# Kernel optimization log

Hardware: AMD Instinct MI355X
Metric: run time of the kernel (lower is better)

## Reference

```python
import jax, jax.numpy as jnp
import numpy as np

DIM = 1024
NUM_HEADS = 16
HEAD_DIM = DIM // NUM_HEADS
BATCH = 64
SEQ = 256


def rope_tables(seq_len, head_dim, dtype=jnp.float32):
    inv_freq = 1.0 / (10000.0 ** (jnp.arange(0, head_dim, 2, dtype=jnp.float32) / head_dim))
    pos = jnp.arange(seq_len, dtype=jnp.float32)
    freqs = jnp.outer(pos, inv_freq)            # (S, head_dim/2)
    emb = jnp.concatenate([freqs, freqs], -1)   # (S, head_dim)
    return jnp.cos(emb).astype(dtype), jnp.sin(emb).astype(dtype)


def rotate_half(x):
    x1, x2 = jnp.split(x, 2, axis=-1)
    return jnp.concatenate([-x2, x1], axis=-1)


def setup_inputs() -> dict:
    key = jax.random.key(0)
    ks = jax.random.split(key, 5)
    x = jax.random.normal(ks[0], (BATCH, SEQ, DIM), dtype=jnp.float32)
    mask = jnp.ones((BATCH, SEQ), dtype=jnp.int32)
    s = 1.0 / np.sqrt(DIM)
    Wq = jax.random.normal(ks[1], (DIM, DIM), dtype=jnp.float32) * s
    Wk = jax.random.normal(ks[2], (DIM, DIM), dtype=jnp.float32) * s
    Wv = jax.random.normal(ks[3], (DIM, DIM), dtype=jnp.float32) * s
    Wo = jax.random.normal(ks[4], (DIM, DIM), dtype=jnp.float32) * s
    return {"x": x, "mask": mask, "Wq": Wq, "Wk": Wk, "Wv": Wv, "Wo": Wo}


def reference(x, mask, Wq, Wk, Wv, Wo):
    B, S, D = x.shape
    H, Hd = NUM_HEADS, HEAD_DIM
    scale = Hd ** -0.5
    # torch nn.Linear: y = x @ W^T  (weights stored as (out,in))
    q = (x @ Wq.T).reshape(B, S, H, Hd).transpose(0, 2, 1, 3)  # (B,H,S,Hd)
    k = (x @ Wk.T).reshape(B, S, H, Hd).transpose(0, 2, 1, 3)
    v = (x @ Wv.T).reshape(B, S, H, Hd).transpose(0, 2, 1, 3)
    cos, sin = rope_tables(S, Hd, x.dtype)       # (S,Hd)
    cos = cos[None, None]                         # (1,1,S,Hd)
    sin = sin[None, None]
    q = q * cos + rotate_half(q) * sin
    k = k * cos + rotate_half(k) * sin
    scores = jnp.einsum('bhqd,bhkd->bhqk', q, k) * scale  # (B,H,S,S)
    m = (mask[:, None, None, :] != 0)             # (B,1,1,S)
    scores = jnp.where(m, scores, -jnp.inf)
    attn = jax.nn.softmax(scores, axis=-1)
    out = jnp.einsum('bhqk,bhkd->bhqd', attn, v)  # (B,H,S,Hd)
    out = out.transpose(0, 2, 1, 3).reshape(B, S, D)
    return out @ Wo.T
```

## Files before the change

### kernel.cpp

```cpp
#include <hip/hip_runtime.h>

typedef __attribute__((ext_vector_type(8))) short short8;
typedef __attribute__((ext_vector_type(4))) float f32x4;

#define DEV __device__ __forceinline__

DEV unsigned short f2bf(float f) {
    unsigned int u = __float_as_uint(f);
    u += 0x7FFFu + ((u >> 16) & 1u);
    return (unsigned short)(u >> 16);
}
DEV float bf2f(unsigned short h) { return __uint_as_float(((unsigned int)h) << 16); }

DEV void gload16(const void* g, void* l) {
    __builtin_amdgcn_global_load_lds(
        (const __attribute__((address_space(1))) void*)(unsigned long long)g,
        (__attribute__((address_space(3))) void*)(unsigned int)(unsigned long long)l,
        16, 0, 0);
}

__global__ void cast_bf16_kernel(const float* __restrict__ in, unsigned short* __restrict__ out, int n8) {
    int gid = blockIdx.x * 256 + threadIdx.x;
    if (gid >= n8) return;
    const f32x4* p = (const f32x4*)in + (size_t)gid * 2;
    f32x4 a = p[0], b = p[1];
    short8 v;
    v[0] = (short)f2bf(a[0]); v[1] = (short)f2bf(a[1]); v[2] = (short)f2bf(a[2]); v[3] = (short)f2bf(a[3]);
    v[4] = (short)f2bf(b[0]); v[5] = (short)f2bf(b[1]); v[6] = (short)f2bf(b[2]); v[7] = (short)f2bf(b[3]);
    *(short8*)(out + (size_t)gid * 8) = v;
}

__global__ void cast_w4_kernel(const float* __restrict__ w0, const float* __restrict__ w1,
                               const float* __restrict__ w2, const float* __restrict__ w3,
                               unsigned short* __restrict__ o0, unsigned short* __restrict__ o1,
                               unsigned short* __restrict__ o2, unsigned short* __restrict__ o3) {
    int gid = blockIdx.x * 256 + threadIdx.x;
    int sel = gid >> 17, idx = gid & 131071;
    const float* in = (sel == 0) ? w0 : (sel == 1) ? w1 : (sel == 2) ? w2 : w3;
    unsigned short* out = (sel == 0) ? o0 : (sel == 1) ? o1 : (sel == 2) ? o2 : o3;
    const f32x4* p = (const f32x4*)in + (size_t)idx * 2;
    f32x4 a = p[0], b = p[1];
    short8 v;
    v[0] = (short)f2bf(a[0]); v[1] = (short)f2bf(a[1]); v[2] = (short)f2bf(a[2]); v[3] = (short)f2bf(a[3]);
    v[4] = (short)f2bf(b[0]); v[5] = (short)f2bf(b[1]); v[6] = (short)f2bf(b[2]); v[7] = (short)f2bf(b[3]);
    *(short8*)(out + (size_t)idx * 8) = v;
}

__global__ void rope_table_kernel(float* __restrict__ cosT, float* __restrict__ sinT) {
    int gid = blockIdx.x * 256 + threadIdx.x;
    if (gid >= 256 * 32) return;
    int s = gid >> 5, i = gid & 31;
    float inv = powf(10000.0f, -(float)i * (1.0f / 32.0f));
    float f = (float)s * inv;
    cosT[gid] = cosf(f);
    sinT[gid] = sinf(f);
}

#define NT 32

#define STAGE(SB, TS) do {                                                     \
    int ts_ = (TS) < NT ? (TS) : (NT - 1);                                     \
    const unsigned short* as_ = Abase + (size_t)ts_ * 32;                      \
    const unsigned short* bs_ = Bbase + (size_t)ts_ * 32;                      \
    gload16(as_ + rel0, &Al[SB][(size_t)tid * 8]);                             \
    gload16(as_ + rel1, &Al[SB][(size_t)(tid + 512) * 8]);                     \
    gload16(bs_ + rel0, &Bl[SB][(size_t)tid * 8]);                             \
    gload16(bs_ + rel1, &Bl[SB][(size_t)(tid + 512) * 8]);                     \
} while (0)

#define RDB(BUF) do {                                                          \
    bv[0] = *(const short8*)&Bl[BUF][boff[0]];                                 \
    bv[1] = *(const short8*)&Bl[BUF][boff[1]];                                 \
    bv[2] = *(const short8*)&Bl[BUF][boff[2]];                                 \
    bv[3] = *(const short8*)&Bl[BUF][boff[3]];                                 \
} while (0)

#define RDA(FR, BUF) do {                                                      \
    FR[0] = *(const short8*)&Al[BUF][aoff[0]];                                 \
    FR[1] = *(const short8*)&Al[BUF][aoff[1]];                                 \
    FR[2] = *(const short8*)&Al[BUF][aoff[2]];                                 \
    FR[3] = *(const short8*)&Al[BUF][aoff[3]];                                 \
    FR[4] = *(const short8*)&Al[BUF][aoff[4]];                                 \
    FR[5] = *(const short8*)&Al[BUF][aoff[5]];                                 \
    FR[6] = *(const short8*)&Al[BUF][aoff[6]];                                 \
    FR[7] = *(const short8*)&Al[BUF][aoff[7]];                                 \
} while (0)

#define MFMA32(F) do {                                                         \
    _Pragma("unroll")                                                          \
    for (int ni = 0; ni < 4; ++ni)                                             \
        _Pragma("unroll")                                                      \
        for (int mi = 0; mi < 8; ++mi)                                         \
            acc[mi][ni] = __builtin_amdgcn_mfma_f32_16x16x32_bf16(             \
                F[mi], bv[ni], acc[mi][ni], 0, 0, 0);                          \
} while (0)

#define TILEB(T, CURB, NXTB, STB, FCUR, FNXT) do {                             \
    RDB(CURB);                                                                 \
    RDA(FNXT, NXTB);                                                           \
    STAGE(STB, (T) + 3);                                                       \
    __builtin_amdgcn_s_setprio(1);                                             \
    MFMA32(FCUR);                                                              \
    __builtin_amdgcn_s_setprio(0);                                             \
    asm volatile("s_waitcnt vmcnt(4)" ::: "memory");                           \
    __builtin_amdgcn_s_barrier();                                              \
    asm volatile("" ::: "memory");                                             \
} while (0)

template <int MODE>
__global__ __launch_bounds__(512, 2) void gemm256_kernel(
    const unsigned short* __restrict__ A,
    const unsigned short* __restrict__ W0,
    const unsigned short* __restrict__ W1,
    const unsigned short* __restrict__ W2,
    unsigned short* __restrict__ q,
    unsigned short* __restrict__ k,
    unsigned short* __restrict__ vt,
    float* __restrict__ outF,
    const float* __restrict__ cosT,
    const float* __restrict__ sinT)
{
    __shared__ __align__(16) unsigned short Al[4][8192];
    __shared__ __align__(16) unsigned short Bl[4][8192];

    const int tid = threadIdx.x;
    const int l = tid & 63;
    const int w = tid >> 6;
    const int wr = w >> 2, wc = w & 3;
    const int l15 = l & 15, lg = l >> 4;

    const int nwg = gridDim.x;
    const int bid = blockIdx.x;
    const int cpx = nwg >> 3;
    const int swz = (bid & 7) * cpx + (bid >> 3);
    const int NBX = (MODE == 0) ? 12 : 4;
    const int bx = swz % NBX, by = swz / NBX;
    const int m0 = by * 256, n0 = bx * 256;

    const unsigned short* Bp;
    int nb, sel = 0;
    if (MODE == 0) {
        sel = n0 >> 10;
        Bp = (sel == 0) ? W0 : ((sel == 1) ? W1 : W2);
        nb = n0 & 1023;
    } else {
        Bp = W0;
        nb = n0;
    }

    const int f0 = tid, f1 = tid + 512;
    const int rel0 = (f0 >> 2) * 1024 + (((f0 & 3) ^ ((f0 >> 3) & 3)) * 8);
    const int rel1 = (f1 >> 2) * 1024 + (((f1 & 3) ^ ((f1 >> 3) & 3)) * 8);
    const unsigned short* Abase = A + (size_t)m0 * 1024;
    const unsigned short* Bbase = Bp + (size_t)nb * 1024;

    int aoff[8], boff[4];
#pragma unroll
    for (int mi = 0; mi < 8; ++mi) {
        int row = wr * 128 + mi * 16 + l15;
        aoff[mi] = row * 32 + ((lg ^ ((row >> 1) & 3)) * 8);
    }
#pragma unroll
    for (int ni = 0; ni < 4; ++ni) {
        int row = wc * 64 + ni * 16 + l15;
        boff[ni] = row * 32 + ((lg ^ ((row >> 1) & 3)) * 8);
    }

    f32x4 acc[8][4];
#pragma unroll
    for (int mi = 0; mi < 8; ++mi)
#pragma unroll
        for (int ni = 0; ni < 4; ++ni)
#pragma unroll
            for (int e = 0; e < 4; ++e) acc[mi][ni][e] = 0.f;

    short8 bv[4], fA[8], fB[8];

    STAGE(0, 0);
    STAGE(1, 1);
    STAGE(2, 2);
    asm volatile("s_waitcnt vmcnt(4)" ::: "memory");
    __builtin_amdgcn_s_barrier();
    asm volatile("" ::: "memory");
    RDA(fA, 0);

#pragma unroll 1
    for (int it = 0; it < NT / 4; ++it) {
        const int t0 = it * 4;
        TILEB(t0 + 0, 0, 1, 3, fA, fB);
        TILEB(t0 + 1, 1, 2, 0, fB, fA);
        TILEB(t0 + 2, 2, 3, 1, fA, fB);
        TILEB(t0 + 3, 3, 0, 2, fB, fA);
    }

    if (MODE == 0) {
#pragma unroll
        for (int mi = 0; mi < 8; ++mi) {
#pragma unroll
            for (int i = 0; i < 4; ++i) {
                int grow = m0 + wr * 128 + mi * 16 + lg * 4 + i;
                int b = grow >> 8, s = grow & 255;
                if (sel < 2) {
#pragma unroll
                    for (int ni = 0; ni < 2; ++ni) {
                        int d = ni * 16 + l15;
                        float c = cosT[s * 32 + d], sn = sinT[s * 32 + d];
                        float lo = acc[mi][ni][i], hi = acc[mi][ni + 2][i];
                        acc[mi][ni][i] = lo * c - hi * sn;
                        acc[mi][ni + 2][i] = hi * c + lo * sn;
                    }
                }
#pragma unroll
                for (int ni = 0; ni < 4; ++ni) {
                    int col = n0 + wc * 64 + ni * 16 + l15;
                    int cc = col & 1023;
                    int h = cc >> 6, d = cc & 63;
                    unsigned short v = f2bf(acc[mi][ni][i]);
                    if (sel == 0)
                        q[((size_t)(b * 16 + h) * 256 + s) * 64 + d] = v;
                    else if (sel == 1)
                        k[((size_t)(b * 16 + h) * 256 + s) * 64 + d] = v;
                    else
                        vt[((size_t)(b * 16 + h) * 64 + d) * 256 + s] = v;
                }
            }
        }
    } else {
#pragma unroll
        for (int mi = 0; mi < 8; ++mi) {
#pragma unroll
            for (int i = 0; i < 4; ++i) {
                int grow = m0 + wr * 128 + mi * 16 + lg * 4 + i;
#pragma unroll
                for (int ni = 0; ni < 4; ++ni) {
                    int col = n0 + wc * 64 + ni * 16 + l15;
                    outF[(size_t)grow * 1024 + col] = acc[mi][ni][i];
                }
            }
        }
    }
}

__global__ __launch_bounds__(512) void attn_kernel(
    const unsigned short* __restrict__ qp,
    const unsigned short* __restrict__ kp,
    const unsigned short* __restrict__ vtp,
    const int* __restrict__ mask,
    unsigned short* __restrict__ ao)
{
    __shared__ __align__(16) unsigned short Ks[128 * 64];
    __shared__ __align__(16) unsigned short Vts[64 * 128];
    __shared__ __align__(16) unsigned short Ps[8][32 * 64];

    const int bh = blockIdx.x;
    const int b = bh >> 4, h = bh & 15;
    const int tid = threadIdx.x;
    const int l = tid & 63, w = tid >> 6;
    const int l15 = l & 15, lg = l >> 4;

    const unsigned short* kbase = kp + (size_t)bh * (256 * 64);
    const unsigned short* vtbase = vtp + (size_t)bh * (64 * 256);
    const unsigned short* qbase = qp + (size_t)bh * (256 * 64) + (size_t)(w * 32) * 64;

    short8 aq[2][2];
#pragma unroll
    for (int m = 0; m < 2; ++m)
#pragma unroll
        for (int ks = 0; ks < 2; ++ks)
            aq[m][ks] = *(const short8*)(qbase + (m * 16 + l15) * 64 + ks * 32 + lg * 8);

    float m_run[2][4], l_run[2][4];
    f32x4 o[2][4];
#pragma unroll
    for (int m = 0; m < 2; ++m)
#pragma unroll
        for (int i = 0; i < 4; ++i) { m_run[m][i] = -3.0e38f; l_run[m][i] = 0.f; }
#pragma unroll
    for (int m = 0; m < 2; ++m)
#pragma unroll
        for (int n = 0; n < 4; ++n)
#pragma unroll
            for (int e = 0; e < 4; ++e) o[m][n][e] = 0.f;

    const int* mrow = mask + b * 256;

    for (int half = 0; half < 2; ++half) {
        __syncthreads();
        for (int c2 = tid; c2 < 1024; c2 += 512) {
            int off = c2 * 16;
            int row = off >> 7, cb = off & 127;
            short8 v = *(const short8*)((const char*)kbase + (size_t)half * 16384 + off);
            *(short8*)((char*)Ks + row * 128 + (cb ^ ((row & 7) << 4))) = v;
        }
        for (int c2 = tid; c2 < 1024; c2 += 512) {
            int off = c2 * 16;
            int row = off >> 8, cb = off & 255;
            short8 v = *(const short8*)((const char*)vtbase + (size_t)row * 512 + half * 256 + cb);
            *(short8*)((char*)Vts + row * 256 + (cb ^ ((row & 7) << 4))) = v;
        }
        __syncthreads();

        for (int t2 = 0; t2 < 2; ++t2) {
            const int keyl = t2 * 64;
            const int keyg = half * 128 + keyl;

            f32x4 sf[2][4];
#pragma unroll
            for (int m = 0; m < 2; ++m)
#pragma unroll
                for (int n = 0; n < 4; ++n)
#pragma unroll
                    for (int e = 0; e < 4; ++e) sf[m][n][e] = 0.f;
#pragma unroll
            for (int ks = 0; ks < 2; ++ks) {
                short8 bk[4];
#pragma unroll
                for (int n = 0; n < 4; ++n) {
                    int row = keyl + n * 16 + l15;
                    int cb = (ks * 64 + lg * 16) ^ ((row & 7) << 4);
                    bk[n] = *(const short8*)((char*)Ks + row * 128 + cb);
                }
#pragma unroll
                for (int m = 0; m < 2; ++m)
#pragma unroll
                    for (int n = 0; n < 4; ++n)
                        sf[m][n] = __builtin_amdgcn_mfma_f32_16x16x32_bf16(aq[m][ks], bk[n], sf[m][n], 0, 0, 0);
            }
            float madd[4];
#pragma unroll
            for (int n = 0; n < 4; ++n) madd[n] = mrow[keyg + n * 16 + l15] ? 0.f : -1e30f;
#pragma unroll
            for (int m = 0; m < 2; ++m)
#pragma unroll
                for (int n = 0; n < 4; ++n)
#pragma unroll
                    for (int i = 0; i < 4; ++i) sf[m][n][i] = sf[m][n][i] * 0.125f + madd[n];
            float al[2][4];
#pragma unroll
            for (int m = 0; m < 2; ++m)
#pragma unroll
                for (int i = 0; i < 4; ++i) {
                    float mx = fmaxf(fmaxf(sf[m][0][i], sf[m][1][i]), fmaxf(sf[m][2][i], sf[m][3][i]));
                    mx = fmaxf(mx, __shfl_xor(mx, 1));
                    mx = fmaxf(mx, __shfl_xor(mx, 2));
                    mx = fmaxf(mx, __shfl_xor(mx, 4));
                    mx = fmaxf(mx, __shfl_xor(mx, 8));
                    float mnew = fmaxf(m_run[m][i], mx);
                    al[m][i] = __expf(m_run[m][i] - mnew);
                    m_run[m][i] = mnew;
                }
            float rs[2][4];
#pragma unroll
            for (int m = 0; m < 2; ++m)
#pragma unroll
                for (int i = 0; i < 4; ++i) rs[m][i] = 0.f;
#pragma unroll
            for (int m = 0; m < 2; ++m)
#pragma unroll
                for (int n = 0; n < 4; ++n)
#pragma unroll
                    for (int i = 0; i < 4; ++i) {
                        float p = __expf(sf[m][n][i] - m_run[m][i]);
                        sf[m][n][i] = p;
                        rs[m][i] += p;
                    }
#pragma unroll
            for (int m = 0; m < 2; ++m)
#pragma unroll
                for (int i = 0; i < 4; ++i) {
                    float r2 = rs[m][i];
                    r2 += __shfl_xor(r2, 1);
                    r2 += __shfl_xor(r2, 2);
                    r2 += __shfl_xor(r2, 4);
                    r2 += __shfl_xor(r2, 8);
                    l_run[m][i] = l_run[m][i] * al[m][i] + r2;
                }
#pragma unroll
            for (int m = 0; m < 2; ++m)
#pragma unroll
                for (int n = 0; n < 4; ++n)
#pragma unroll
                    for (int i = 0; i < 4; ++i) o[m][n][i] *= al[m][i];

            __syncthreads();
#pragma unroll
            for (int m = 0; m < 2; ++m)
#pragma unroll
                for (int n = 0; n < 4; ++n)
#pragma unroll
                    for (int i = 0; i < 4; ++i) {
                        int row = m * 16 + lg * 4 + i;
                        int cb = ((n * 16 + l15) * 2) ^ ((row & 7) << 4);
                        *(unsigned short*)((char*)Ps[w] + row * 128 + cb) = f2bf(sf[m][n][i]);
                    }
            __syncthreads();
#pragma unroll
            for (int ks = 0; ks < 2; ++ks) {
                short8 pa[2];
#pragma unroll
                for (int m = 0; m < 2; ++m) {
                    int row = m * 16 + l15;
                    int cb = (ks * 64 + lg * 16) ^ ((row & 7) << 4);
                    pa[m] = *(const short8*)((char*)Ps[w] + row * 128 + cb);
                }
                short8 vb[4];
#pragma unroll
                for (int n = 0; n < 4; ++n) {
                    int row = n * 16 + l15;
                    int cb = (keyl * 2 + ks * 64 + lg * 16) ^ ((row & 7) << 4);
                    vb[n] = *(const short8*)((char*)Vts + row * 256 + cb);
                }
#pragma unroll
                for (int m = 0; m < 2; ++m)
#pragma unroll
                    for (int n = 0; n < 4; ++n)
                        o[m][n] = __builtin_amdgcn_mfma_f32_16x16x32_bf16(pa[m], vb[n], o[m][n], 0, 0, 0);
            }
        }
    }

    unsigned short* aop = ao + ((size_t)(b * 256 + w * 32)) * 1024 + h * 64;
#pragma unroll
    for (int m = 0; m < 2; ++m)
#pragma unroll
        for (int n = 0; n < 4; ++n)
#pragma unroll
            for (int i = 0; i < 4; ++i) {
                int row = m * 16 + lg * 4 + i;
                int d = n * 16 + l15;
                aop[(size_t)row * 1024 + d] = f2bf(o[m][n][i] / l_run[m][i]);
            }
}

extern "C" void kernel_launch(void* const* d_in, const int* in_sizes, int n_in,
                              void* d_out, int out_size, void* d_ws, size_t ws_size,
                              hipStream_t stream) {
    const float* x = (const float*)d_in[0];
    const int* mask = (const int*)d_in[1];
    const float* Wq = (const float*)d_in[2];
    const float* Wk = (const float*)d_in[3];
    const float* Wv = (const float*)d_in[4];
    const float* Wo = (const float*)d_in[5];
    float* out = (float*)d_out;

    char* ws = (char*)d_ws;
    size_t off = 0;
    auto alloc = [&](size_t bytes) -> char* {
        char* p = ws + off;
        off = (off + bytes + 255) & ~(size_t)255;
        return p;
    };
    unsigned short* xb = (unsigned short*)alloc((size_t)16384 * 1024 * 2);
    unsigned short* wqb = (unsigned short*)alloc((size_t)1024 * 1024 * 2);
    unsigned short* wkb = (unsigned short*)alloc((size_t)1024 * 1024 * 2);
    unsigned short* wvb = (unsigned short*)alloc((size_t)1024 * 1024 * 2);
    unsigned short* wob = (unsigned short*)alloc((size_t)1024 * 1024 * 2);
    unsigned short* q = (unsigned short*)alloc((size_t)16384 * 1024 * 2);
    unsigned short* k = (unsigned short*)alloc((size_t)16384 * 1024 * 2);
    unsigned short* vt = (unsigned short*)alloc((size_t)16384 * 1024 * 2);
    float* cosT = (float*)alloc(256 * 32 * 4);
    float* sinT = (float*)alloc(256 * 32 * 4);

    cast_bf16_kernel<<<16777216 / 8 / 256, 256, 0, stream>>>(x, xb, 16777216 / 8);
    cast_w4_kernel<<<4 * 131072 / 256, 256, 0, stream>>>(Wq, Wk, Wv, Wo, wqb, wkb, wvb, wob);
    rope_table_kernel<<<32, 256, 0, stream>>>(cosT, sinT);

    gemm256_kernel<0><<<768, 512, 0, stream>>>(xb, wqb, wkb, wvb, q, k, vt, nullptr, cosT, sinT);
    attn_kernel<<<1024, 512, 0, stream>>>(q, k, vt, mask, xb );
    gemm256_kernel<1><<<256, 512, 0, stream>>>(xb, wob, nullptr, nullptr, nullptr, nullptr, nullptr, out, nullptr, nullptr);

    (void)in_sizes; (void)n_in; (void)out_size; (void)ws_size;
}
```

Measured before the change: 298.7 us.

## Restructure GEMM main loop into two half-tile phases with prefetch depth two

The GEMM K-loop now splits each K-tile into two phases of sixteen MFMAs each. Each phase reads half of the A fragments (plus B in the first phase) from LDS, issues the global-to-LDS load for only the A or only the B half of a future tile, and synchronises with barriers and sched_barrier fences. Prefetch depth drops from three tiles ahead to two, and the fB register double-buffer is removed, which cuts VGPR pressure. This interleaves memory issue with compute more finely, at the cost of extra barriers per tile and a shallower prefetch.

```diff
diff --git a/kernel.cpp b/kernel.cpp
--- a/kernel.cpp
+++ b/kernel.cpp
@@ -58,53 +58,59 @@
 
 #define NT 32
 
-#define STAGE(SB, TS) do {                                                     \
+#define RD16(ARR, OFF) (*(const short8*)&(ARR)[OFF])
+
+#define STG(DST, BASEP, TS) do {                                               \
     int ts_ = (TS) < NT ? (TS) : (NT - 1);                                     \
-    const unsigned short* as_ = Abase + (size_t)ts_ * 32;                      \
-    const unsigned short* bs_ = Bbase + (size_t)ts_ * 32;                      \
-    gload16(as_ + rel0, &Al[SB][(size_t)tid * 8]);                             \
-    gload16(as_ + rel1, &Al[SB][(size_t)(tid + 512) * 8]);                     \
-    gload16(bs_ + rel0, &Bl[SB][(size_t)tid * 8]);                             \
-    gload16(bs_ + rel1, &Bl[SB][(size_t)(tid + 512) * 8]);                     \
+    const unsigned short* sp_ = (BASEP) + (size_t)ts_ * 32;                    \
+    gload16(sp_ + rel0, &(DST)[(size_t)tid * 8]);                              \
+    gload16(sp_ + rel1, &(DST)[(size_t)(tid + 512) * 8]);                      \
 } while (0)
 
-#define RDB(BUF) do {                                                          \
-    bv[0] = *(const short8*)&Bl[BUF][boff[0]];                                 \
-    bv[1] = *(const short8*)&Bl[BUF][boff[1]];                                 \
-    bv[2] = *(const short8*)&Bl[BUF][boff[2]];                                 \
-    bv[3] = *(const short8*)&Bl[BUF][boff[3]];                                 \
+#define MM4(MI, A) do {                                                        \
+    acc[MI][0] = __builtin_amdgcn_mfma_f32_16x16x32_bf16(A, bv[0], acc[MI][0], 0, 0, 0); \
+    acc[MI][1] = __builtin_amdgcn_mfma_f32_16x16x32_bf16(A, bv[1], acc[MI][1], 0, 0, 0); \
+    acc[MI][2] = __builtin_amdgcn_mfma_f32_16x16x32_bf16(A, bv[2], acc[MI][2], 0, 0, 0); \
+    acc[MI][3] = __builtin_amdgcn_mfma_f32_16x16x32_bf16(A, bv[3], acc[MI][3], 0, 0, 0); \
 } while (0)
 
-#define RDA(FR, BUF) do {                                                      \
-    FR[0] = *(const short8*)&Al[BUF][aoff[0]];                                 \
-    FR[1] = *(const short8*)&Al[BUF][aoff[1]];                                 \
-    FR[2] = *(const short8*)&Al[BUF][aoff[2]];                                 \
-    FR[3] = *(const short8*)&Al[BUF][aoff[3]];                                 \
-    FR[4] = *(const short8*)&Al[BUF][aoff[4]];                                 \
-    FR[5] = *(const short8*)&Al[BUF][aoff[5]];                                 \
-    FR[6] = *(const short8*)&Al[BUF][aoff[6]];                                 \
-    FR[7] = *(const short8*)&Al[BUF][aoff[7]];                                 \
+#define PHA(BUF, SBUF, TS) do {                                                \
+    short8 a0 = RD16(Al[BUF], aoff[0]);                                        \
+    short8 a1 = RD16(Al[BUF], aoff[1]);                                        \
+    short8 a2 = RD16(Al[BUF], aoff[2]);                                        \
+    short8 a3 = RD16(Al[BUF], aoff[3]);                                        \
+    bv[0] = RD16(Bl[BUF], boff[0]);                                            \
+    bv[1] = RD16(Bl[BUF], boff[1]);                                            \
+    bv[2] = RD16(Bl[BUF], boff[2]);                                            \
+    bv[3] = RD16(Bl[BUF], boff[3]);                                            \
+    STG(Al[SBUF], Abase, TS);                                                  \
+    __builtin_amdgcn_sched_barrier(0);                                         \
+    __builtin_amdgcn_s_barrier();                                              \
+    asm volatile("s_waitcnt lgkmcnt(0)" ::: "memory");                         \
+    __builtin_amdgcn_sched_barrier(0);                                         \
+    __builtin_amdgcn_s_setprio(1);                                             \
+    MM4(0, a0); MM4(1, a1); MM4(2, a2); MM4(3, a3);                            \
+    __builtin_amdgcn_s_setprio(0);                                             \
+    __builtin_amdgcn_sched_barrier(0);                                         \
+    __builtin_amdgcn_s_barrier();                                              \
 } while (0)
 
-#define MFMA32(F) do {                                                         \
-    _Pragma("unroll")                                                          \
-    for (int ni = 0; ni < 4; ++ni)                                             \
-        _Pragma("unroll")                                                      \
-        for (int mi = 0; mi < 8; ++mi)                                         \
-            acc[mi][ni] = __builtin_amdgcn_mfma_f32_16x16x32_bf16(             \
-                F[mi], bv[ni], acc[mi][ni], 0, 0, 0);                          \
-} while (0)
-
-#define TILEB(T, CURB, NXTB, STB, FCUR, FNXT) do {                             \
-    RDB(CURB);                                                                 \
-    RDA(FNXT, NXTB);                                                           \
-    STAGE(STB, (T) + 3);                                                       \
+#define PHB(BUF, SBUF, TS) do {                                                \
+    short8 a4 = RD16(Al[BUF], aoff[4]);                                        \
+    short8 a5 = RD16(Al[BUF], aoff[5]);                                        \
+    short8 a6 = RD16(Al[BUF], aoff[6]);                                        \
+    short8 a7 = RD16(Al[BUF], aoff[7]);                                        \
+    STG(Bl[SBUF], Bbase, TS);                                                  \
+    __builtin_amdgcn_sched_barrier(0);                                         \
+    __builtin_amdgcn_s_barrier();                                              \
+    asm volatile("s_waitcnt lgkmcnt(0)" ::: "memory");                         \
+    __builtin_amdgcn_sched_barrier(0);                                         \
     __builtin_amdgcn_s_setprio(1);                                             \
-    MFMA32(FCUR);                                                              \
+    MM4(4, a4); MM4(5, a5); MM4(6, a6); MM4(7, a7);                            \
     __builtin_amdgcn_s_setprio(0);                                             \
     asm volatile("s_waitcnt vmcnt(4)" ::: "memory");                           \
+    __builtin_amdgcn_sched_barrier(0);                                         \
     __builtin_amdgcn_s_barrier();                                              \
-    asm volatile("" ::: "memory");                                             \
 } while (0)
 
 template <int MODE>
@@ -174,23 +180,21 @@
 #pragma unroll
             for (int e = 0; e < 4; ++e) acc[mi][ni][e] = 0.f;
 
-    short8 bv[4], fA[8], fB[8];
-
-    STAGE(0, 0);
-    STAGE(1, 1);
-    STAGE(2, 2);
+    short8 bv[4];
+
+    STG(Al[0], Abase, 0); STG(Bl[0], Bbase, 0);
+    STG(Al[1], Abase, 1); STG(Bl[1], Bbase, 1);
     asm volatile("s_waitcnt vmcnt(4)" ::: "memory");
+    __builtin_amdgcn_sched_barrier(0);
     __builtin_amdgcn_s_barrier();
-    asm volatile("" ::: "memory");
-    RDA(fA, 0);
 
 #pragma unroll 1
     for (int it = 0; it < NT / 4; ++it) {
         const int t0 = it * 4;
-        TILEB(t0 + 0, 0, 1, 3, fA, fB);
-        TILEB(t0 + 1, 1, 2, 0, fB, fA);
-        TILEB(t0 + 2, 2, 3, 1, fA, fB);
-        TILEB(t0 + 3, 3, 0, 2, fB, fA);
+        PHA(0, 2, t0 + 2); PHB(0, 2, t0 + 2);
+        PHA(1, 3, t0 + 3); PHB(1, 3, t0 + 3);
+        PHA(2, 0, t0 + 4); PHB(2, 0, t0 + 4);
+        PHA(3, 1, t0 + 5); PHB(3, 1, t0 + 5);
     }
 
     if (MODE == 0) {
```

New measurement: 301.2 us. Within noise of the previous version (+0.8%).
